# Optimization experiments

Measured on AMD Instinct MI355X. Metric: run time of the kernel, lower is better.

## Reference

```python
import jax, jax.numpy as jnp
import numpy as np

B, S, E, D = 32, 2048, 1024, 1024


def setup_inputs() -> dict:
    key = jax.random.key(0)
    k0, k1, k2, k3, k4 = jax.random.split(key, 5)
    scale_e = 1.0 / np.sqrt(E)
    scale_d = 1.0 / np.sqrt(D)
    return {
        "hidden": jax.random.normal(k0, (B, D), dtype=jnp.float32),
        "encoder_outputs": jax.random.normal(k1, (S, B, E), dtype=jnp.float32),
        "We": jax.random.normal(k2, (D, E), dtype=jnp.float32) * scale_e,
        "Wd": jax.random.normal(k3, (D, D), dtype=jnp.float32) * scale_d,
        "v": jax.random.normal(k4, (D,), dtype=jnp.float32) * scale_d,
    }


def reference(hidden, encoder_outputs, We, Wd, v):
    # encoder projection: [S,B,E] x [D,E] -> [B,S,D] (batch-first for the add)
    enc_proj = jnp.einsum("sbe,de->bsd", encoder_outputs, We)
    # decoder projection broadcast over src positions: [B,1,D]
    dec_proj = (hidden @ Wd.T)[:, None, :]
    energy = jnp.tanh(enc_proj + dec_proj)          # [B,S,D]
    scores = jnp.einsum("bsd,d->bs", energy, v)     # v-layer, squeeze(-1)
    attention_weights = jax.nn.softmax(scores, axis=1)  # softmax over src_len
    # weighted sum of encoder outputs: bmm([B,1,S],[B,S,E]) -> [B,E]
    context = jnp.einsum("bs,sbe->be", attention_weights, encoder_outputs)
    return context, attention_weights
```

## Files before the change

kernel.cpp:

```cpp
#include <hip/hip_runtime.h>
#include <cmath>
#include <cstdint>

constexpr int B_ = 32;
constexpr int S_ = 2048;
constexpr int E_ = 1024;
constexpr int D_ = 1024;
constexpr int K_ = E_;
constexpr int M_ = S_ * B_;
constexpr int SC_ = 32;
constexpr int NP_ = 16;

typedef float f32x4 __attribute__((ext_vector_type(4)));
typedef float fvec4 __attribute__((ext_vector_type(4)));
typedef __bf16 bf16x8 __attribute__((ext_vector_type(8)));

__device__ __forceinline__ float fast_tanh(float x) {
    float e = __builtin_amdgcn_exp2f(x * 2.88539008177793f);
    return 1.f - 2.f * __builtin_amdgcn_rcpf(e + 1.f);
}

__device__ __forceinline__ uint16_t f2bf(float f) {
    uint32_t u = __float_as_uint(f);
    u += 0x7FFFu + ((u >> 16) & 1u);
    return (uint16_t)(u >> 16);
}

constexpr int ENC_N8 = M_ * K_ / 8;
constexpr int WE_N8  = D_ * K_ / 8;
constexpr int CVT_BLOCKS = (ENC_N8 + WE_N8) / 256;
constexpr int DEC_BLOCKS = (B_ * D_) / 4;

__global__ __launch_bounds__(256) void prep_kernel(
    const float* __restrict__ enc, uint16_t* __restrict__ encb,
    const float* __restrict__ We,  uint16_t* __restrict__ Web,
    const float* __restrict__ hidden, const float* __restrict__ Wd,
    float* __restrict__ dec)
{
    const int bid = blockIdx.x;
    if (bid < CVT_BLOCKS) {
        int tid = bid * 256 + threadIdx.x;
        const float* src;
        uint16_t* dst;
        int i8;
        if (tid < ENC_N8) { src = enc; dst = encb; i8 = tid; }
        else              { src = We;  dst = Web;  i8 = tid - ENC_N8; }
        const fvec4* s4 = reinterpret_cast<const fvec4*>(src) + (size_t)i8 * 2;
        fvec4 a = __builtin_nontemporal_load(s4);
        fvec4 b = __builtin_nontemporal_load(s4 + 1);
        uint4 o;
        o.x = (uint32_t)f2bf(a.x) | ((uint32_t)f2bf(a.y) << 16);
        o.y = (uint32_t)f2bf(a.z) | ((uint32_t)f2bf(a.w) << 16);
        o.z = (uint32_t)f2bf(b.x) | ((uint32_t)f2bf(b.y) << 16);
        o.w = (uint32_t)f2bf(b.z) | ((uint32_t)f2bf(b.w) << 16);
        reinterpret_cast<uint4*>(dst)[i8] = o;
    } else {
        const int o = (bid - CVT_BLOCKS) * 4 + (threadIdx.x >> 6);
        const int lane = threadIdx.x & 63;
        const int b = o >> 10;
        const int d = o & (D_ - 1);
        const float4* h4 = reinterpret_cast<const float4*>(hidden + (size_t)b * D_);
        const float4* w4 = reinterpret_cast<const float4*>(Wd + (size_t)d * D_);
        float acc = 0.f;
#pragma unroll
        for (int p = 0; p < 4; ++p) {
            float4 h = h4[lane + p * 64], w = w4[lane + p * 64];
            acc += h.x * w.x + h.y * w.y + h.z * w.z + h.w * w.w;
        }
#pragma unroll
        for (int off = 32; off > 0; off >>= 1) acc += __shfl_xor(acc, off);
        if (lane == 0) dec[o] = acc;
    }
}

constexpr int TM = 128, TN = 128;

__global__ __launch_bounds__(256) void score_mfma_kernel(
    const uint16_t* __restrict__ A,
    const uint16_t* __restrict__ Bw,
    const float* __restrict__ dec,
    const float* __restrict__ v,
    float* __restrict__ spart)
{
    __shared__ __align__(16) uint16_t As[2][TM * 32];
    __shared__ __align__(16) uint16_t Bs[2][TN * 32];

    const int p    = blockIdx.x;
    const int xcd  = p & 7;
    const int slot = p >> 3;
    const int nb   = slot & 7;
    const int mb   = xcd + 8 * (slot >> 3);
    const int m0 = mb * TM;
    const int n0 = nb * TN;

    const int t    = threadIdx.x;
    const int wave = t >> 6;
    const int lane = t & 63;
    const int wm   = (wave & 1) * 64;
    const int wn   = (wave >> 1) * 64;
    const int q    = lane >> 4;
    const int r16  = lane & 15;

    const int srow = lane >> 2;
    const int scol = (lane & 3) * 8;

    const int c0 = wave * 2, c1 = wave * 2 + 1;
    const uint16_t* ga00 = A + (size_t)(m0 + c0 * 16 + srow) * K_ + scol;
    const uint16_t* ga01 = ga00 + 32;
    const uint16_t* ga10 = A + (size_t)(m0 + c1 * 16 + srow) * K_ + scol;
    const uint16_t* ga11 = ga10 + 32;
    const uint16_t* gb00 = Bw + (size_t)(n0 + c0 * 16 + srow) * K_ + scol;
    const uint16_t* gb01 = gb00 + 32;
    const uint16_t* gb10 = Bw + (size_t)(n0 + c1 * 16 + srow) * K_ + scol;
    const uint16_t* gb11 = gb10 + 32;
    typedef __attribute__((address_space(3))) uint32_t lds_u32;
    typedef const __attribute__((address_space(1))) uint32_t g_u32;
    lds_u32* dA00 = (lds_u32*)(As[0] + c0 * 512);
    lds_u32* dA01 = (lds_u32*)(As[1] + c0 * 512);
    lds_u32* dA10 = (lds_u32*)(As[0] + c1 * 512);
    lds_u32* dA11 = (lds_u32*)(As[1] + c1 * 512);
    lds_u32* dB00 = (lds_u32*)(Bs[0] + c0 * 512);
    lds_u32* dB01 = (lds_u32*)(Bs[1] + c0 * 512);
    lds_u32* dB10 = (lds_u32*)(Bs[0] + c1 * 512);
    lds_u32* dB11 = (lds_u32*)(Bs[1] + c1 * 512);

    float vj[4];
#pragma unroll
    for (int j = 0; j < 4; ++j) vj[j] = v[n0 + wn + j * 16 + r16];
    float dec_r[2][4][4];
#pragma unroll
    for (int i01 = 0; i01 < 2; ++i01)
#pragma unroll
        for (int r = 0; r < 4; ++r) {
            const int b = i01 * 16 + q * 4 + r;
#pragma unroll
            for (int j = 0; j < 4; ++j)
                dec_r[i01][r][j] = dec[b * D_ + n0 + wn + j * 16 + r16];
        }

    f32x4 acc[4][4] = {};

    for (int it = 0; it < K_ / 64; ++it) {
        __syncthreads();
        __builtin_amdgcn_global_load_lds((g_u32*)ga00, dA00, 16, 0, 0);
        __builtin_amdgcn_global_load_lds((g_u32*)ga01, dA01, 16, 0, 0);
        __builtin_amdgcn_global_load_lds((g_u32*)ga10, dA10, 16, 0, 0);
        __builtin_amdgcn_global_load_lds((g_u32*)ga11, dA11, 16, 0, 0);
        __builtin_amdgcn_global_load_lds((g_u32*)gb00, dB00, 16, 0, 0);
        __builtin_amdgcn_global_load_lds((g_u32*)gb01, dB01, 16, 0, 0);
        __builtin_amdgcn_global_load_lds((g_u32*)gb10, dB10, 16, 0, 0);
        __builtin_amdgcn_global_load_lds((g_u32*)gb11, dB11, 16, 0, 0);
        ga00 += 64; ga01 += 64; ga10 += 64; ga11 += 64;
        gb00 += 64; gb01 += 64; gb10 += 64; gb11 += 64;
        __syncthreads();

#pragma unroll
        for (int h = 0; h < 2; ++h) {
            bf16x8 af[4], bf[4];
#pragma unroll
            for (int i = 0; i < 4; ++i) {
                af[i] = __builtin_bit_cast(bf16x8,
                    *reinterpret_cast<const int4*>(As[h] + (wm + i * 16 + r16) * 32 + q * 8));
                bf[i] = __builtin_bit_cast(bf16x8,
                    *reinterpret_cast<const int4*>(Bs[h] + (wn + i * 16 + r16) * 32 + q * 8));
            }
#pragma unroll
            for (int i = 0; i < 4; ++i)
#pragma unroll
                for (int j = 0; j < 4; ++j)
                    acc[i][j] = __builtin_amdgcn_mfma_f32_16x16x32_bf16(
                        af[i], bf[j], acc[i][j], 0, 0, 0);
        }
    }

    float* plane = spart + (size_t)(nb * 2 + (wn >> 6)) * M_;

#pragma unroll
    for (int i = 0; i < 4; ++i) {
#pragma unroll
        for (int r = 0; r < 4; ++r) {
            const int m = m0 + wm + i * 16 + q * 4 + r;
            const int b = (i & 1) * 16 + q * 4 + r;
            float pv = 0.f;
#pragma unroll
            for (int j = 0; j < 4; ++j)
                pv += vj[j] * fast_tanh(acc[i][j][r] + dec_r[i & 1][r][j]);
            pv += __shfl_xor(pv, 1);
            pv += __shfl_xor(pv, 2);
            pv += __shfl_xor(pv, 4);
            pv += __shfl_xor(pv, 8);
            if (r16 == 0) plane[b * S_ + (m >> 5)] = pv;
        }
    }
}

__global__ __launch_bounds__(256) void softmax16_kernel(
    const float* __restrict__ spart,
    float* __restrict__ attn)
{
    const int b = blockIdx.x;
    const int t = threadIdx.x;
    __shared__ float sm[256];

    const float4* base = reinterpret_cast<const float4*>(spart + (size_t)b * S_);
    constexpr int PSTRIDE = M_ / 4;
    float4 v0 = {0, 0, 0, 0}, v1 = {0, 0, 0, 0};
#pragma unroll
    for (int p = 0; p < NP_; ++p) {
        float4 a = base[(size_t)p * PSTRIDE + t];
        float4 c = base[(size_t)p * PSTRIDE + t + 256];
        v0.x += a.x; v0.y += a.y; v0.z += a.z; v0.w += a.w;
        v1.x += c.x; v1.y += c.y; v1.z += c.z; v1.w += c.w;
    }

    float lmax = fmaxf(fmaxf(fmaxf(v0.x, v0.y), fmaxf(v0.z, v0.w)),
                       fmaxf(fmaxf(v1.x, v1.y), fmaxf(v1.z, v1.w)));
    sm[t] = lmax; __syncthreads();
    for (int off = 128; off > 0; off >>= 1) {
        if (t < off) sm[t] = fmaxf(sm[t], sm[t + off]);
        __syncthreads();
    }
    const float mx = sm[0];
    __syncthreads();

    v0.x = __builtin_amdgcn_exp2f((v0.x - mx) * 1.44269504f);
    v0.y = __builtin_amdgcn_exp2f((v0.y - mx) * 1.44269504f);
    v0.z = __builtin_amdgcn_exp2f((v0.z - mx) * 1.44269504f);
    v0.w = __builtin_amdgcn_exp2f((v0.w - mx) * 1.44269504f);
    v1.x = __builtin_amdgcn_exp2f((v1.x - mx) * 1.44269504f);
    v1.y = __builtin_amdgcn_exp2f((v1.y - mx) * 1.44269504f);
    v1.z = __builtin_amdgcn_exp2f((v1.z - mx) * 1.44269504f);
    v1.w = __builtin_amdgcn_exp2f((v1.w - mx) * 1.44269504f);

    float lsum = v0.x + v0.y + v0.z + v0.w + v1.x + v1.y + v1.z + v1.w;
    sm[t] = lsum; __syncthreads();
    for (int off = 128; off > 0; off >>= 1) {
        if (t < off) sm[t] += sm[t + off];
        __syncthreads();
    }
    const float inv = 1.f / sm[0];
    float4* op = reinterpret_cast<float4*>(attn + (size_t)b * S_);
    v0.x *= inv; v0.y *= inv; v0.z *= inv; v0.w *= inv;
    v1.x *= inv; v1.y *= inv; v1.z *= inv; v1.w *= inv;
    op[t] = v0; op[t + 256] = v1;
}

__global__ __launch_bounds__(256) void context_part_kernel(
    const uint16_t* __restrict__ encb, const float* __restrict__ attn,
    float* __restrict__ part)
{
    const int b  = blockIdx.x & (B_ - 1);
    const int sc = blockIdx.x >> 5;
    const int e0 = threadIdx.x * 4;
    constexpr int SLEN = S_ / SC_;

    float a0 = 0.f, a1 = 0.f, a2 = 0.f, a3 = 0.f;
    const int s0 = sc * SLEN;
#pragma unroll 2
    for (int s = s0; s < s0 + SLEN; ++s) {
        const float w = attn[b * S_ + s];
        uint2 u = *reinterpret_cast<const uint2*>(
            encb + ((size_t)s * B_ + b) * E_ + e0);
        a0 += w * __uint_as_float((u.x & 0xFFFFu) << 16);
        a1 += w * __uint_as_float(u.x & 0xFFFF0000u);
        a2 += w * __uint_as_float((u.y & 0xFFFFu) << 16);
        a3 += w * __uint_as_float(u.y & 0xFFFF0000u);
    }
    float4 o = {a0, a1, a2, a3};
    *reinterpret_cast<float4*>(part + ((size_t)sc * B_ + b) * E_ + e0) = o;
}

__global__ __launch_bounds__(256) void context_reduce_kernel(
    const float* __restrict__ part, float* __restrict__ ctx)
{
    const int i = blockIdx.x * 256 + threadIdx.x;
    float acc = 0.f;
#pragma unroll
    for (int sc = 0; sc < SC_; ++sc) acc += part[(size_t)sc * B_ * E_ + i];
    ctx[i] = acc;
}

constexpr int BM = 64, BN = 64, BK = 16;

__global__ __launch_bounds__(256) void dec_proj_wave_kernel(
    const float* __restrict__ hidden, const float* __restrict__ Wd,
    float* __restrict__ dec)
{
    const int o = blockIdx.x * 4 + (threadIdx.x >> 6);
    const int lane = threadIdx.x & 63;
    const int b = o >> 10;
    const int d = o & (D_ - 1);
    const float4* h4 = reinterpret_cast<const float4*>(hidden + (size_t)b * D_);
    const float4* w4 = reinterpret_cast<const float4*>(Wd + (size_t)d * D_);
    float acc = 0.f;
#pragma unroll
    for (int p = 0; p < 4; ++p) {
        float4 h = h4[lane + p * 64], w = w4[lane + p * 64];
        acc += h.x * w.x + h.y * w.y + h.z * w.z + h.w * w.w;
    }
#pragma unroll
    for (int off = 32; off > 0; off >>= 1) acc += __shfl_xor(acc, off);
    if (lane == 0) dec[o] = acc;
}

__global__ __launch_bounds__(256) void score_gemm_kernel(
    const float* __restrict__ enc, const float* __restrict__ We,
    const float* __restrict__ dec, const float* __restrict__ v,
    float* __restrict__ scores)
{
    __shared__ float As[BM][BK + 1];
    __shared__ float Bs[BN][BK + 1];
    __shared__ float red[BM][17];
    const int m0 = blockIdx.x * BM;
    const int n0 = blockIdx.y * BN;
    const int t  = threadIdx.x;
    const int tx = t & 15;
    const int ty = t >> 4;
    const int lrow = t >> 2;
    const int lcol = (t & 3) * 4;
    float acc[4][4] = {};
    for (int k0 = 0; k0 < E_; k0 += BK) {
        float4 a = *reinterpret_cast<const float4*>(enc + (size_t)(m0 + lrow) * E_ + k0 + lcol);
        float4 w = *reinterpret_cast<const float4*>(We + (size_t)(n0 + lrow) * E_ + k0 + lcol);
        As[lrow][lcol + 0] = a.x; As[lrow][lcol + 1] = a.y;
        As[lrow][lcol + 2] = a.z; As[lrow][lcol + 3] = a.w;
        Bs[lrow][lcol + 0] = w.x; Bs[lrow][lcol + 1] = w.y;
        Bs[lrow][lcol + 2] = w.z; Bs[lrow][lcol + 3] = w.w;
        __syncthreads();
#pragma unroll
        for (int kk = 0; kk < BK; ++kk) {
            float av[4], bw[4];
#pragma unroll
            for (int i = 0; i < 4; ++i) av[i] = As[ty * 4 + i][kk];
#pragma unroll
            for (int j = 0; j < 4; ++j) bw[j] = Bs[tx * 4 + j][kk];
#pragma unroll
            for (int i = 0; i < 4; ++i)
#pragma unroll
                for (int j = 0; j < 4; ++j)
                    acc[i][j] += av[i] * bw[j];
        }
        __syncthreads();
    }
    float pp[4];
#pragma unroll
    for (int i = 0; i < 4; ++i) {
        int m = m0 + ty * 4 + i;
        int b = m & (B_ - 1);
        float s = 0.f;
#pragma unroll
        for (int j = 0; j < 4; ++j) {
            int n = n0 + tx * 4 + j;
            s += v[n] * tanhf(acc[i][j] + dec[b * D_ + n]);
        }
        pp[i] = s;
    }
#pragma unroll
    for (int i = 0; i < 4; ++i) red[ty * 4 + i][tx] = pp[i];
    __syncthreads();
    if (t < BM) {
        float s = 0.f;
#pragma unroll
        for (int j = 0; j < 16; ++j) s += red[t][j];
        atomicAdd(&scores[m0 + t], s);
    }
}

__global__ __launch_bounds__(256) void softmax_kernel(
    const float* __restrict__ scores, float* __restrict__ attn)
{
    const int b = blockIdx.x;
    const int t = threadIdx.x;
    __shared__ float sm[256];
    float vals[8];
    float lmax = -INFINITY;
#pragma unroll
    for (int i = 0; i < 8; ++i) {
        int s = t + i * 256;
        vals[i] = scores[s * B_ + b];
        lmax = fmaxf(lmax, vals[i]);
    }
    sm[t] = lmax; __syncthreads();
    for (int off = 128; off > 0; off >>= 1) {
        if (t < off) sm[t] = fmaxf(sm[t], sm[t + off]);
        __syncthreads();
    }
    const float mx = sm[0];
    __syncthreads();
    float lsum = 0.f;
#pragma unroll
    for (int i = 0; i < 8; ++i) {
        vals[i] = expf(vals[i] - mx);
        lsum += vals[i];
    }
    sm[t] = lsum; __syncthreads();
    for (int off = 128; off > 0; off >>= 1) {
        if (t < off) sm[t] += sm[t + off];
        __syncthreads();
    }
    const float inv = 1.f / sm[0];
#pragma unroll
    for (int i = 0; i < 8; ++i)
        attn[b * S_ + t + i * 256] = vals[i] * inv;
}

__global__ __launch_bounds__(256) void context_kernel(
    const float* __restrict__ enc, const float* __restrict__ attn,
    float* __restrict__ ctx)
{
    const int e0 = (blockIdx.x & 3) * 256;
    const int b  = (blockIdx.x >> 2) & (B_ - 1);
    const int sc = blockIdx.x >> 7;
    const int e  = e0 + threadIdx.x;
    float acc = 0.f;
    const int s_end = sc * 256 + 256;
    for (int s = sc * 256; s < s_end; ++s)
        acc += attn[b * S_ + s] * enc[((size_t)s * B_ + b) * E_ + e];
    atomicAdd(&ctx[b * E_ + e], acc);
}

extern "C" void kernel_launch(void* const* d_in, const int* in_sizes, int n_in,
                              void* d_out, int out_size, void* d_ws, size_t ws_size,
                              hipStream_t stream) {
    const float* hidden = (const float*)d_in[0];
    const float* enc    = (const float*)d_in[1];
    const float* We     = (const float*)d_in[2];
    const float* Wd     = (const float*)d_in[3];
    const float* v      = (const float*)d_in[4];

    float* ctx  = (float*)d_out;
    float* attn = (float*)d_out + B_ * E_;

    float*    dec   = (float*)d_ws;
    float*    spart = dec + B_ * D_;
    uint16_t* Web   = (uint16_t*)(spart + (size_t)NP_ * M_);
    uint16_t* encb  = Web + (size_t)D_ * K_;

    const size_t need = (size_t)B_ * D_ * 4 + (size_t)NP_ * M_ * 4
                      + ((size_t)D_ * K_ + (size_t)M_ * K_) * 2;
    const bool fast = ws_size >= need;

    if (fast) {
        prep_kernel<<<CVT_BLOCKS + DEC_BLOCKS, 256, 0, stream>>>(
            enc, encb, We, Web, hidden, Wd, dec);

        score_mfma_kernel<<<(M_ / TM) * (D_ / TN), 256, 0, stream>>>(
            encb, Web, dec, v, spart);

        softmax16_kernel<<<B_, 256, 0, stream>>>(spart, attn);
        context_part_kernel<<<SC_ * B_, 256, 0, stream>>>(encb, attn, spart);
        context_reduce_kernel<<<(B_ * E_) / 256, 256, 0, stream>>>(spart, ctx);
    } else {
        float* scores = spart;
        hipMemsetAsync(scores, 0, (size_t)M_ * sizeof(float), stream);
        hipMemsetAsync(ctx, 0, (size_t)B_ * E_ * sizeof(float), stream);
        dec_proj_wave_kernel<<<(B_ * D_) / 4, 256, 0, stream>>>(hidden, Wd, dec);
        dim3 g2(M_ / BM, D_ / BN);
        score_gemm_kernel<<<g2, 256, 0, stream>>>(enc, We, dec, v, scores);
        softmax_kernel<<<B_, 256, 0, stream>>>(scores, attn);
        context_kernel<<<B_ * 4 * 8, 256, 0, stream>>>(enc, attn, ctx);
    }
}
```

Measured before the change: 563.4 us.

## Rewrite score GEMM with 256x256 tiles, 4-stage LDS pipeline and swizzle

The score GEMM kernel moves from 128x128 tiles with 256 threads and a double-buffered synchronous loop to 256x256 tiles with 512 threads. Global-to-LDS loads now run through a four-buffer ring with explicit vmcnt waits, and LDS addresses are XOR-swizzled to avoid bank conflicts. MFMA phases are interleaved with staging and raised in priority through setprio. The goal is more data reuse per block and memory latency hidden behind compute, at the cost of higher register and LDS pressure and tricky manual waitcnt correctness.

```diff
diff --git a/kernel.cpp b/kernel.cpp
--- a/kernel.cpp
+++ b/kernel.cpp
@@ -14,6 +14,8 @@
 typedef float f32x4 __attribute__((ext_vector_type(4)));
 typedef float fvec4 __attribute__((ext_vector_type(4)));
 typedef __bf16 bf16x8 __attribute__((ext_vector_type(8)));
+typedef __attribute__((address_space(3))) uint32_t lds_u32;
+typedef const __attribute__((address_space(1))) uint32_t g_u32;
 
 __device__ __forceinline__ float fast_tanh(float x) {
     float e = __builtin_amdgcn_exp2f(x * 2.88539008177793f);
@@ -73,60 +75,148 @@
     }
 }
 
-constexpr int TM = 128, TN = 128;
-
-__global__ __launch_bounds__(256) void score_mfma_kernel(
+constexpr int TM2 = 256, TN2 = 256, TK2 = 32;
+constexpr int NT2 = K_ / TK2;
+constexpr int TILE_B = TM2 * TK2 * 2;
+constexpr int BUF_B  = TILE_B * 2;
+
+#define TILE_STEP(T, DO_STAGE)                                                \
+  do {                                                                        \
+    const int buf_ = (T) & 3;                                                 \
+    const char* bufA_ = ldsc + buf_ * BUF_B;                                  \
+    const char* bufB_ = bufA_ + TILE_B;                                       \
+    bf16x8 a0_[4], bv_[4];                                                    \
+    _Pragma("unroll")                                                         \
+    for (int i = 0; i < 4; ++i)                                               \
+      a0_[i] = __builtin_bit_cast(bf16x8,                                     \
+          *reinterpret_cast<const int4*>(bufA_ + offA[i]));                   \
+    _Pragma("unroll")                                                         \
+    for (int j = 0; j < 4; ++j)                                               \
+      bv_[j] = __builtin_bit_cast(bf16x8,                                     \
+          *reinterpret_cast<const int4*>(bufB_ + offB[j]));                   \
+    if (DO_STAGE) {                                                           \
+      char* sb_ = ldsc + (((T) + 3) & 3) * BUF_B;                             \
+      __builtin_amdgcn_global_load_lds((g_u32*)pA0, (lds_u32*)(sb_ + dst0), 16, 0, 0); \
+      __builtin_amdgcn_global_load_lds((g_u32*)pA1, (lds_u32*)(sb_ + dst1), 16, 0, 0); \
+      pA0 += TK2; pA1 += TK2;                                                 \
+    }                                                                         \
+    __builtin_amdgcn_s_barrier();                                             \
+    asm volatile("s_waitcnt lgkmcnt(0)" ::: "memory");                        \
+    __builtin_amdgcn_sched_barrier(0);                                        \
+    __builtin_amdgcn_s_setprio(1);                                            \
+    _Pragma("unroll")                                                         \
+    for (int i = 0; i < 4; ++i)                                               \
+      _Pragma("unroll")                                                       \
+      for (int j = 0; j < 4; ++j)                                             \
+        acc[i][j] = __builtin_amdgcn_mfma_f32_16x16x32_bf16(                  \
+            a0_[i], bv_[j], acc[i][j], 0, 0, 0);                              \
+    __builtin_amdgcn_s_setprio(0);                                            \
+    __builtin_amdgcn_s_barrier();                                             \
+    bf16x8 a1_[4];                                                            \
+    _Pragma("unroll")                                                         \
+    for (int i = 0; i < 4; ++i)                                               \
+      a1_[i] = __builtin_bit_cast(bf16x8,                                     \
+          *reinterpret_cast<const int4*>(bufA_ + offA[4 + i]));               \
+    if (DO_STAGE) {                                                           \
+      char* sb_ = ldsc + (((T) + 3) & 3) * BUF_B + TILE_B;                    \
+      __builtin_amdgcn_global_load_lds((g_u32*)pB0, (lds_u32*)(sb_ + dst0), 16, 0, 0); \
+      __builtin_amdgcn_global_load_lds((g_u32*)pB1, (lds_u32*)(sb_ + dst1), 16, 0, 0); \
+      pB0 += TK2; pB1 += TK2;                                                 \
+    }                                                                         \
+    __builtin_amdgcn_s_barrier();                                             \
+    asm volatile("s_waitcnt lgkmcnt(0)" ::: "memory");                        \
+    __builtin_amdgcn_sched_barrier(0);                                        \
+    __builtin_amdgcn_s_setprio(1);                                            \
+    _Pragma("unroll")                                                         \
+    for (int i = 0; i < 4; ++i)                                               \
+      _Pragma("unroll")                                                       \
+      for (int j = 0; j < 4; ++j)                                             \
+        acc[4 + i][j] = __builtin_amdgcn_mfma_f32_16x16x32_bf16(              \
+            a1_[i], bv_[j], acc[4 + i][j], 0, 0, 0);                          \
+    __builtin_amdgcn_s_setprio(0);                                            \
+  } while (0)
+
+__global__ __launch_bounds__(512, 2) void score_mfma_kernel(
     const uint16_t* __restrict__ A,
     const uint16_t* __restrict__ Bw,
     const float* __restrict__ dec,
     const float* __restrict__ v,
     float* __restrict__ spart)
 {
-    __shared__ __align__(16) uint16_t As[2][TM * 32];
-    __shared__ __align__(16) uint16_t Bs[2][TN * 32];
+    __shared__ __align__(16) uint16_t smem[4 * 2 * TM2 * TK2];
 
     const int p    = blockIdx.x;
     const int xcd  = p & 7;
     const int slot = p >> 3;
-    const int nb   = slot & 7;
-    const int mb   = xcd + 8 * (slot >> 3);
-    const int m0 = mb * TM;
-    const int n0 = nb * TN;
-
-    const int t    = threadIdx.x;
-    const int wave = t >> 6;
-    const int lane = t & 63;
-    const int wm   = (wave & 1) * 64;
-    const int wn   = (wave >> 1) * 64;
+    const int nb   = slot & 3;
+    const int mb   = xcd + 8 * (slot >> 2);
+    const int m0 = mb * TM2;
+    const int n0 = nb * TN2;
+
+    const int tid  = threadIdx.x;
+    const int wave = tid >> 6;
+    const int lane = tid & 63;
+    const int wm   = wave >> 2;
+    const int wn   = wave & 3;
     const int q    = lane >> 4;
     const int r16  = lane & 15;
 
-    const int srow = lane >> 2;
-    const int scol = (lane & 3) * 8;
-
-    const int c0 = wave * 2, c1 = wave * 2 + 1;
-    const uint16_t* ga00 = A + (size_t)(m0 + c0 * 16 + srow) * K_ + scol;
-    const uint16_t* ga01 = ga00 + 32;
-    const uint16_t* ga10 = A + (size_t)(m0 + c1 * 16 + srow) * K_ + scol;
-    const uint16_t* ga11 = ga10 + 32;
-    const uint16_t* gb00 = Bw + (size_t)(n0 + c0 * 16 + srow) * K_ + scol;
-    const uint16_t* gb01 = gb00 + 32;
-    const uint16_t* gb10 = Bw + (size_t)(n0 + c1 * 16 + srow) * K_ + scol;
-    const uint16_t* gb11 = gb10 + 32;
-    typedef __attribute__((address_space(3))) uint32_t lds_u32;
-    typedef const __attribute__((address_space(1))) uint32_t g_u32;
-    lds_u32* dA00 = (lds_u32*)(As[0] + c0 * 512);
-    lds_u32* dA01 = (lds_u32*)(As[1] + c0 * 512);
-    lds_u32* dA10 = (lds_u32*)(As[0] + c1 * 512);
-    lds_u32* dA11 = (lds_u32*)(As[1] + c1 * 512);
-    lds_u32* dB00 = (lds_u32*)(Bs[0] + c0 * 512);
-    lds_u32* dB01 = (lds_u32*)(Bs[1] + c0 * 512);
-    lds_u32* dB10 = (lds_u32*)(Bs[0] + c1 * 512);
-    lds_u32* dB11 = (lds_u32*)(Bs[1] + c1 * 512);
+    char* ldsc = (char*)smem;
+
+    int offA[8], offB[4];
+#pragma unroll
+    for (int i = 0; i < 8; ++i) {
+        const int r = wm * 128 + i * 16 + r16;
+        offA[i] = (r * 64 + q * 16) ^ ((r & 7) << 4);
+    }
+#pragma unroll
+    for (int j = 0; j < 4; ++j) {
+        const int r = wn * 64 + j * 16 + r16;
+        offB[j] = (r * 64 + q * 16) ^ ((r & 7) << 4);
+    }
+
+    const int l2     = lane >> 2;
+    const int bbit   = (lane >> 4) & 1;
+    const int rowSwz = l2 ^ bbit;
+    const int gsel   = (lane & 3) ^ (rowSwz & 3);
+    const uint16_t* pA0 = A  + (size_t)(m0 + wave * 32 +  0 + rowSwz) * K_ + gsel * 8;
+    const uint16_t* pA1 = A  + (size_t)(m0 + wave * 32 + 16 + rowSwz) * K_ + gsel * 8;
+    const uint16_t* pB0 = Bw + (size_t)(n0 + wave * 32 +  0 + rowSwz) * K_ + gsel * 8;
+    const uint16_t* pB1 = Bw + (size_t)(n0 + wave * 32 + 16 + rowSwz) * K_ + gsel * 8;
+    const int dst0 = wave * 2048;
+    const int dst1 = dst0 + 1024;
+
+#pragma unroll
+    for (int tt = 0; tt < 3; ++tt) {
+        char* sb = ldsc + tt * BUF_B;
+        __builtin_amdgcn_global_load_lds((g_u32*)pA0, (lds_u32*)(sb + dst0), 16, 0, 0);
+        __builtin_amdgcn_global_load_lds((g_u32*)pA1, (lds_u32*)(sb + dst1), 16, 0, 0);
+        __builtin_amdgcn_global_load_lds((g_u32*)pB0, (lds_u32*)(sb + TILE_B + dst0), 16, 0, 0);
+        __builtin_amdgcn_global_load_lds((g_u32*)pB1, (lds_u32*)(sb + TILE_B + dst1), 16, 0, 0);
+        pA0 += TK2; pA1 += TK2; pB0 += TK2; pB1 += TK2;
+    }
+    asm volatile("s_waitcnt vmcnt(8)" ::: "memory");
+    __builtin_amdgcn_s_barrier();
+
+    f32x4 acc[8][4] = {};
+
+#pragma unroll 1
+    for (int t = 0; t < NT2 - 3; ++t) {
+        TILE_STEP(t, true);
+        asm volatile("s_waitcnt vmcnt(8)" ::: "memory");
+        __builtin_amdgcn_s_barrier();
+    }
+    TILE_STEP(NT2 - 3, false);
+    asm volatile("s_waitcnt vmcnt(4)" ::: "memory");
+    __builtin_amdgcn_s_barrier();
+    TILE_STEP(NT2 - 2, false);
+    asm volatile("s_waitcnt vmcnt(0)" ::: "memory");
+    __builtin_amdgcn_s_barrier();
+    TILE_STEP(NT2 - 1, false);
 
     float vj[4];
 #pragma unroll
-    for (int j = 0; j < 4; ++j) vj[j] = v[n0 + wn + j * 16 + r16];
+    for (int j = 0; j < 4; ++j) vj[j] = v[n0 + wn * 64 + j * 16 + r16];
     float dec_r[2][4][4];
 #pragma unroll
     for (int i01 = 0; i01 < 2; ++i01)
@@ -135,51 +225,16 @@
             const int b = i01 * 16 + q * 4 + r;
 #pragma unroll
             for (int j = 0; j < 4; ++j)
-                dec_r[i01][r][j] = dec[b * D_ + n0 + wn + j * 16 + r16];
+                dec_r[i01][r][j] = dec[b * D_ + n0 + wn * 64 + j * 16 + r16];
         }
 
-    f32x4 acc[4][4] = {};
-
-    for (int it = 0; it < K_ / 64; ++it) {
-        __syncthreads();
-        __builtin_amdgcn_global_load_lds((g_u32*)ga00, dA00, 16, 0, 0);
-        __builtin_amdgcn_global_load_lds((g_u32*)ga01, dA01, 16, 0, 0);
-        __builtin_amdgcn_global_load_lds((g_u32*)ga10, dA10, 16, 0, 0);
-        __builtin_amdgcn_global_load_lds((g_u32*)ga11, dA11, 16, 0, 0);
-        __builtin_amdgcn_global_load_lds((g_u32*)gb00, dB00, 16, 0, 0);
-        __builtin_amdgcn_global_load_lds((g_u32*)gb01, dB01, 16, 0, 0);
-        __builtin_amdgcn_global_load_lds((g_u32*)gb10, dB10, 16, 0, 0);
-        __builtin_amdgcn_global_load_lds((g_u32*)gb11, dB11, 16, 0, 0);
-        ga00 += 64; ga01 += 64; ga10 += 64; ga11 += 64;
-        gb00 += 64; gb01 += 64; gb10 += 64; gb11 += 64;
-        __syncthreads();
-
-#pragma unroll
-        for (int h = 0; h < 2; ++h) {
-            bf16x8 af[4], bf[4];
-#pragma unroll
-            for (int i = 0; i < 4; ++i) {
-                af[i] = __builtin_bit_cast(bf16x8,
-                    *reinterpret_cast<const int4*>(As[h] + (wm + i * 16 + r16) * 32 + q * 8));
-                bf[i] = __builtin_bit_cast(bf16x8,
-                    *reinterpret_cast<const int4*>(Bs[h] + (wn + i * 16 + r16) * 32 + q * 8));
-            }
-#pragma unroll
-            for (int i = 0; i < 4; ++i)
-#pragma unroll
-                for (int j = 0; j < 4; ++j)
-                    acc[i][j] = __builtin_amdgcn_mfma_f32_16x16x32_bf16(
-                        af[i], bf[j], acc[i][j], 0, 0, 0);
-        }
-    }
-
-    float* plane = spart + (size_t)(nb * 2 + (wn >> 6)) * M_;
-
-#pragma unroll
-    for (int i = 0; i < 4; ++i) {
+    float* plane = spart + (size_t)(nb * 4 + wn) * M_;
+
+#pragma unroll
+    for (int i = 0; i < 8; ++i) {
 #pragma unroll
         for (int r = 0; r < 4; ++r) {
-            const int m = m0 + wm + i * 16 + q * 4 + r;
+            const int m = m0 + wm * 128 + i * 16 + q * 4 + r;
             const int b = (i & 1) * 16 + q * 4 + r;
             float pv = 0.f;
 #pragma unroll
@@ -444,7 +499,7 @@
         prep_kernel<<<CVT_BLOCKS + DEC_BLOCKS, 256, 0, stream>>>(
             enc, encb, We, Web, hidden, Wd, dec);
 
-        score_mfma_kernel<<<(M_ / TM) * (D_ / TN), 256, 0, stream>>>(
+        score_mfma_kernel<<<(M_ / TM2) * (D_ / TN2), 512, 0, stream>>>(
             encb, Web, dec, v, spart);
 
         softmax16_kernel<<<B_, 256, 0, stream>>>(spart, attn);
```

After: 541.9 us. 1.04x faster.
